# Kernel optimization log

Hardware: AMD Instinct MI355X
Metric: run time of the kernel (lower is better)

## Reference

```python
import jax, jax.numpy as jnp
import numpy as np

B, C, H, W, K = 32, 256, 32, 32, 1024
BETA = 0.25

def setup_inputs() -> dict:
    key = jax.random.key(0)
    k1, k2 = jax.random.split(key)
    z = jax.random.normal(k1, (B, C, H, W), dtype=jnp.float32)
    # torch init: uniform(-1/K, 1/K)
    embedding = jax.random.uniform(k2, (K, C), dtype=jnp.float32,
                                   minval=-1.0 / K, maxval=1.0 / K)
    return {"z": z, "embedding": embedding}

def reference(z, embedding):
    b, c, h, w = z.shape
    k = embedding.shape[0]
    # permute to [b,h,w,c] (contiguous)
    z_p = jnp.transpose(z, (0, 2, 3, 1))
    # Faithful to the torch code: the [b,h,w,c] contiguous buffer is .view()'d
    # as [b,1,c,h,w]; numpy/jnp reshape of the transposed array matches that.
    zz = z_p.reshape(b, c, h * w)                     # [b,c,hw] (reinterpreted)
    e = jax.lax.stop_gradient(embedding)              # torch uses .data here
    # ||e - z||^2 via dot-product trick, avoids [b,k,c,h,w] intermediate
    dist = (jnp.sum(e * e, axis=1)[None, :, None]
            + jnp.sum(zz * zz, axis=1)[:, None, :]
            - 2.0 * jnp.einsum('kc,bcn->bkn', e, zz))  # [b,k,hw]
    idx = jnp.argmin(dist, axis=1).reshape(b, h, w)    # [b,h,w]
    z_q = embedding[idx]                               # [b,h,w,c]
    loss = (jnp.mean((jax.lax.stop_gradient(z_q) - z_p) ** 2)
            + BETA * jnp.mean((z_q - jax.lax.stop_gradient(z_p)) ** 2))
    # straight-through estimator
    z_q_st = z_p + jax.lax.stop_gradient(z_q - z_p)
    return jnp.transpose(z_q_st, (0, 3, 1, 2)), idx, loss
```

## Files before the change

### kernel.cpp

```cpp
#include <hip/hip_runtime.h>
#include <stdint.h>

#define ZSIZE   8388608
#define NPIX    32768
#define IDX_OFF ZSIZE
#define LOSS_OFF (ZSIZE + NPIX)
#define ET_OFF  1024
#define E1_OFF  263168
#define ZT_OFF  394240
#define SZ_OFF  4588544
#define CAP     24
#define WWIN    6.0e-3f

using v8s = __attribute__((ext_vector_type(8))) short;
using v4f = __attribute__((ext_vector_type(4))) float;

__device__ __forceinline__ unsigned short bf16rne(float f) {
  unsigned u = __float_as_uint(f);
  return (unsigned short)((u + 0x7FFFu + ((u >> 16) & 1u)) >> 16);
}

__global__ __launch_bounds__(256) void ktr(const float* __restrict__ E,
                                           float* __restrict__ out) {
  __shared__ float tile[64][65];
  const int k0 = blockIdx.x * 64;
  const int c0 = blockIdx.y * 64;
  const int t = threadIdx.x;
  #pragma unroll
  for (int i = 0; i < 4; i++) {
    int f = t + 256 * i;
    int r = f >> 4, q = f & 15;
    float4 e = *(const float4*)(E + (k0 + r) * 256 + c0 + 4 * q);
    tile[r][4 * q + 0] = e.x; tile[r][4 * q + 1] = e.y;
    tile[r][4 * q + 2] = e.z; tile[r][4 * q + 3] = e.w;
  }
  __syncthreads();
  #pragma unroll
  for (int i = 0; i < 4; i++) {
    int f = t + 256 * i;
    int cr = f >> 4, kq = f & 15;
    float4 o;
    o.x = tile[4 * kq + 0][cr];
    o.y = tile[4 * kq + 1][cr];
    o.z = tile[4 * kq + 2][cr];
    o.w = tile[4 * kq + 3][cr];
    *(float4*)(out + ET_OFF + (c0 + cr) * 1024 + k0 + 4 * kq) = o;
  }
}

__global__ __launch_bounds__(256) void kse(float* __restrict__ out) {
  const int k = blockIdx.x * 256 + threadIdx.x;
  const float* Et = out + ET_OFF;
  float acc = 0.0f;
  #pragma unroll 8
  for (int c = 0; c < 256; c++) {
    float v = Et[c * 1024 + k];
    acc = __fadd_rn(acc, __fmul_rn(v, v));
  }
  out[k] = acc;
}

__global__ __launch_bounds__(256) void kes(const float* __restrict__ E,
                                           float* __restrict__ out) {
  unsigned short* e1s = (unsigned short*)(out + E1_OFF);
  const int tile = blockIdx.x;
  const int t = threadIdx.x;
  #pragma unroll
  for (int i = 0; i < 2; i++) {
    int chunk = t + 256 * i;
    int s = chunk >> 6, lane = chunk & 63;
    int r = lane & 15, h = (lane >> 4) & 3;
    const float* src = E + (16 * tile + r) * 256 + 8 * h + 32 * s;
    unsigned short o[8];
    #pragma unroll
    for (int j = 0; j < 8; j++) o[j] = bf16rne(src[j]);
    *(uint4*)(e1s + (size_t)tile * 4096 + (size_t)chunk * 8) = *(const uint4*)o;
  }
}

__global__ __launch_bounds__(256) void kzt(const float* __restrict__ z,
                                           float* __restrict__ out) {
  __shared__ float tile[16][1028];
  unsigned short* zt = (unsigned short*)(out + ZT_OFF);
  float* szg = out + SZ_OFF;
  const int mg = blockIdx.x;
  const int b  = blockIdx.y;
  const int t = threadIdx.x;
  #pragma unroll
  for (int i = 0; i < 16; i++) {
    float4 v = *(const float4*)(z + (size_t)b * 262144 + (size_t)(mg * 16 + i) * 1024 + 4 * t);
    *(float4*)&tile[i][4 * t] = v;
  }
  __syncthreads();
  const int m = t & 15, w0 = (t >> 4) & 3;
  const int n = w0 * 256 + mg * 16 + m;
  #pragma unroll
  for (int i = 0; i < 8; i++) {
    int g = 4 * i + (t >> 6);
    int c0 = 8 * g;
    unsigned short o[8];
    #pragma unroll
    for (int j = 0; j < 8; j++)
      o[j] = bf16rne(tile[m][4 * (c0 + j) + w0]);
    *(uint4*)(zt + ((size_t)(b * 1024 + n)) * 256 + c0) = *(const uint4*)o;
  }
  if (t < 64) {
    const int ms = t >> 2, ws = t & 3;
    float a = 0.0f;
    #pragma unroll 8
    for (int c = 0; c < 256; c++) {
      float v = tile[ms][4 * c + ws];
      a = __fadd_rn(a, __fmul_rn(v, v));
    }
    szg[b * 1024 + ws * 256 + mg * 16 + ms] = a;
  }
}

__global__ __launch_bounds__(512, 2) void kmain(const float* __restrict__ z,
                                                const float* __restrict__ E,
                                                float* __restrict__ out) {
  __shared__ __attribute__((aligned(16))) float szs[64];
  __shared__ __attribute__((aligned(16))) float dmins[64];
  __shared__ int   candK[64 * CAP];
  __shared__ float candD[64 * CAP];
  __shared__ int   cnt[64];

  const int t = threadIdx.x;
  const int ccg = blockIdx.x, b = blockIdx.y;
  const int cc0 = ccg * 16;
  const int lane = t & 63;
  const int w = (t >> 6) & 3;
  const int Tp = t >> 8;
  const int r = t & 15, h = (t >> 4) & 3;
  const int w16r = w * 16 + r;
  const float* zb = z + (size_t)b * 262144;
  const float* se_g = out;
  const unsigned short* e1s = (const unsigned short*)(out + E1_OFF);
  const unsigned short* zt = (const unsigned short*)(out + ZT_OFF);
  const float* szg = out + SZ_OFF;

  if (t < 64) {
    cnt[t] = 0; dmins[t] = 3.4e38f;
    szs[t] = szg[b * 1024 + (t & 3) * 256 + cc0 + (t >> 2)];
  }
  __syncthreads();

  float se16r[16];
  #pragma unroll
  for (int ti = 0; ti < 16; ti++) se16r[ti] = se_g[ti * 64 + w16r];

  const int T0 = 2 * Tp, T1 = T0 + 1;

  v8s A0[8], A1[8];
  {
    const unsigned short* a0p =
        zt + ((size_t)(b * 1024 + T0 * 256 + cc0 + r)) * 256 + 8 * h;
    const unsigned short* a1p = a0p + 256 * 256;
    #pragma unroll
    for (int s = 0; s < 8; s++) {
      A0[s] = *(const v8s*)(a0p + 32 * s);
      A1[s] = *(const v8s*)(a1p + 32 * s);
    }
  }
  float sz0[4], sz1[4];
  #pragma unroll
  for (int reg = 0; reg < 4; reg++) {
    sz0[reg] = szs[16 * h + 4 * reg + T0];
    sz1[reg] = szs[16 * h + 4 * reg + T1];
  }

  {
    float b0[4], b1[4];
    #pragma unroll
    for (int reg = 0; reg < 4; reg++) { b0[reg] = 3.4e38f; b1[reg] = 3.4e38f; }

    #pragma unroll 4
    for (int ti = 0; ti < 16; ti++) {
      const unsigned short* bb = e1s + (size_t)(4 * ti + w) * 4096 + (size_t)lane * 8;
      v4f acc0 = (v4f){0.f, 0.f, 0.f, 0.f};
      v4f acc1 = (v4f){0.f, 0.f, 0.f, 0.f};
      #pragma unroll
      for (int s = 0; s < 8; s++) {
        v8s B_ = *(const v8s*)(bb + 512 * s);
        acc0 = __builtin_amdgcn_mfma_f32_16x16x32_bf16(A0[s], B_, acc0, 0, 0, 0);
        acc1 = __builtin_amdgcn_mfma_f32_16x16x32_bf16(A1[s], B_, acc1, 0, 0, 0);
      }
      float se_l = se16r[ti];
      #pragma unroll
      for (int reg = 0; reg < 4; reg++) {
        b0[reg] = fminf(b0[reg], (se_l + sz0[reg]) - 2.0f * acc0[reg]);
        b1[reg] = fminf(b1[reg], (se_l + sz1[reg]) - 2.0f * acc1[reg]);
      }
    }
    #pragma unroll
    for (int reg = 0; reg < 4; reg++) {
      atomicMin((int*)&dmins[16 * h + 4 * reg + T0], __float_as_int(b0[reg]));
      atomicMin((int*)&dmins[16 * h + 4 * reg + T1], __float_as_int(b1[reg]));
    }
  }
  __syncthreads();

  {
    float th0[4], th1[4];
    #pragma unroll
    for (int reg = 0; reg < 4; reg++) {
      th0[reg] = dmins[16 * h + 4 * reg + T0] + WWIN;
      th1[reg] = dmins[16 * h + 4 * reg + T1] + WWIN;
    }

    #pragma unroll 4
    for (int ti = 0; ti < 16; ti++) {
      const unsigned short* bb = e1s + (size_t)(4 * ti + w) * 4096 + (size_t)lane * 8;
      v4f acc0 = (v4f){0.f, 0.f, 0.f, 0.f};
      v4f acc1 = (v4f){0.f, 0.f, 0.f, 0.f};
      #pragma unroll
      for (int s = 0; s < 8; s++) {
        v8s B_ = *(const v8s*)(bb + 512 * s);
        acc0 = __builtin_amdgcn_mfma_f32_16x16x32_bf16(A0[s], B_, acc0, 0, 0, 0);
        acc1 = __builtin_amdgcn_mfma_f32_16x16x32_bf16(A1[s], B_, acc1, 0, 0, 0);
      }
      float se_l = se16r[ti];
      const int kl = ti * 64 + w16r;
      #pragma unroll
      for (int reg = 0; reg < 4; reg++) {
        float dd0 = (se_l + sz0[reg]) - 2.0f * acc0[reg];
        if (dd0 <= th0[reg]) {
          int p = 16 * h + 4 * reg + T0;
          int o = atomicAdd(&cnt[p], 1);
          if (o < CAP) { candK[p * CAP + o] = kl; candD[p * CAP + o] = dd0; }
        }
        float dd1 = (se_l + sz1[reg]) - 2.0f * acc1[reg];
        if (dd1 <= th1[reg]) {
          int p = 16 * h + 4 * reg + T1;
          int o = atomicAdd(&cnt[p], 1);
          if (o < CAP) { candK[p * CAP + o] = kl; candD[p * CAP + o] = dd1; }
        }
      }
    }
  }
  __syncthreads();

  for (int i = t; i < 64 * CAP; i += 512) {
    int p = i / CAP, slot = i - p * CAP;
    int cn = cnt[p];
    if (cn > CAP || slot >= cn) continue;
    int k = candK[i];
    const float* er = E + (size_t)k * 256;
    const float* zp = zb + (cc0 + (p >> 2)) * 1024 + (p & 3);
    float dot = 0.0f;
    #pragma unroll 8
    for (int c = 0; c < 256; c++)
      dot = __fmaf_rn(zp[4 * c], er[c], dot);
    candD[i] = __fsub_rn(__fadd_rn(se_g[k], szs[p]), __fmul_rn(2.0f, dot));
  }
  __syncthreads();

  if (t < 64) {
    int p = t, cn = cnt[p];
    if (cn <= CAP) {
      float bd = 3.4e38f; int bi = 0x7FFFFFFF;
      for (int s2 = 0; s2 < cn; s2++) {
        float d2 = candD[p * CAP + s2]; int k2 = candK[p * CAP + s2];
        if (d2 < bd || (d2 == bd && k2 < bi)) { bd = d2; bi = k2; }
      }
      int rr = p >> 2, w0 = p & 3;
      out[IDX_OFF + b * 1024 + (w0 * 256 + cc0 + rr)] = (float)bi;
    }
  }

  for (int p = 0; p < 64; p++) {
    if (cnt[p] > CAP && (p & 3) == w && Tp == 0) {
      const float* zp = zb + (cc0 + (p >> 2)) * 1024 + (p & 3);
      float bd = 3.4e38f; int bi = 0x7FFFFFFF;
      for (int k = lane; k < 1024; k += 64) {
        const float* er = E + (size_t)k * 256;
        float dot = 0.0f;
        #pragma unroll 8
        for (int c = 0; c < 256; c++)
          dot = __fmaf_rn(zp[4 * c], er[c], dot);
        float d2 = __fsub_rn(__fadd_rn(se_g[k], szs[p]), __fmul_rn(2.0f, dot));
        if (d2 < bd || (d2 == bd && k < bi)) { bd = d2; bi = k; }
      }
      #pragma unroll
      for (int mm = 32; mm >= 1; mm >>= 1) {
        float d2 = __shfl_xor(bd, mm, 64);
        int i2 = __shfl_xor(bi, mm, 64);
        if (d2 < bd || (d2 == bd && i2 < bi)) { bd = d2; bi = i2; }
      }
      if (lane == 0) {
        int rr = p >> 2, w0 = p & 3;
        out[IDX_OFF + b * 1024 + (w0 * 256 + cc0 + rr)] = (float)bi;
      }
    }
  }
}

__global__ __launch_bounds__(256) void kout(const float* __restrict__ z,
                                            const float* __restrict__ E,
                                            float* __restrict__ out,
                                            float* __restrict__ ws) {
  __shared__ float red[4];
  const int t = threadIdx.x;
  const size_t g4 = (size_t)blockIdx.x * 256 + t;
  const size_t g = g4 * 4;
  const int b = (int)(g >> 18);
  const int c = (int)((g >> 10) & 255);
  const int n = (int)(g & 1023);

  float4 zp = *(const float4*)(z + g);
  float4 idxf = *(const float4*)(out + IDX_OFF + b * 1024 + n);
  int i0 = (int)idxf.x, i1 = (int)idxf.y, i2 = (int)idxf.z, i3 = (int)idxf.w;
  float q0 = E[i0 * 256 + c];
  float q1 = E[i1 * 256 + c];
  float q2 = E[i2 * 256 + c];
  float q3 = E[i3 * 256 + c];
  float d0 = __fsub_rn(q0, zp.x);
  float d1 = __fsub_rn(q1, zp.y);
  float d2 = __fsub_rn(q2, zp.z);
  float d3 = __fsub_rn(q3, zp.w);
  float4 o;
  o.x = __fadd_rn(zp.x, d0);
  o.y = __fadd_rn(zp.y, d1);
  o.z = __fadd_rn(zp.z, d2);
  o.w = __fadd_rn(zp.w, d3);
  *(float4*)(out + g) = o;

  float s = d0 * d0 + d1 * d1 + d2 * d2 + d3 * d3;
  #pragma unroll
  for (int off = 32; off > 0; off >>= 1) s += __shfl_down(s, off);
  if ((t & 63) == 0) red[t >> 6] = s;
  __syncthreads();
  if (t == 0) ws[blockIdx.x] = red[0] + red[1] + red[2] + red[3];
}

__global__ __launch_bounds__(256) void kfin(const float* __restrict__ ws,
                                            float* __restrict__ out) {
  __shared__ float red[4];
  const int t = threadIdx.x;
  float s = 0.0f;
  #pragma unroll
  for (int i = 0; i < 32; i++) s += ws[t + 256 * i];
  #pragma unroll
  for (int off = 32; off > 0; off >>= 1) s += __shfl_down(s, off);
  if ((t & 63) == 0) red[t >> 6] = s;
  __syncthreads();
  if (t == 0) {
    float S = red[0] + red[1] + red[2] + red[3];
    float m = S / 8388608.0f;
    out[LOSS_OFF] = __fadd_rn(m, __fmul_rn(0.25f, m));
  }
}

extern "C" void kernel_launch(void* const* d_in, const int* in_sizes, int n_in,
                              void* d_out, int out_size, void* d_ws, size_t ws_size,
                              hipStream_t stream) {
  const float* z = (const float*)d_in[0];
  const float* E = (const float*)d_in[1];
  float* out = (float*)d_out;
  float* ws = (float*)d_ws;

  ktr<<<dim3(16, 4), 256, 0, stream>>>(E, out);
  kse<<<dim3(4), 256, 0, stream>>>(out);
  kes<<<dim3(64), 256, 0, stream>>>(E, out);
  kzt<<<dim3(16, 32), 256, 0, stream>>>(z, out);
  kmain<<<dim3(16, 32), 512, 0, stream>>>(z, E, out);
  kout<<<dim3(8192), 256, 0, stream>>>(z, E, out, ws);
  kfin<<<dim3(1), 256, 0, stream>>>(ws, out);
}
```

Before: 305.5 us.

## Cache quantized distances in LDS instead of recomputing MFMA pass for candidate filtering

The main VQ kernel previously ran the bf16 MFMA distance GEMM twice, once for the per-pixel minimum and once to collect candidates. It now stores each distance, minus the pixel norm and quantized to 16 bits, into a large LDS array during the first pass, then filters candidates from those cached values after the min reduction. Each block drops to 256 threads and loops over the two pixel-pair groups, and the codebook tile order is rotated per block to spread L2 traffic. This removes half the MFMA and codebook-load work, but adds about 66KB of LDS per block, which may limit occupancy, and adds quantization error covered by an extra margin.

```diff
diff --git a/kernel.cpp b/kernel.cpp
--- a/kernel.cpp
+++ b/kernel.cpp
@@ -11,6 +11,7 @@
 #define SZ_OFF  4588544
 #define CAP     24
 #define WWIN    6.0e-3f
+#define QMARG   1.5e-4f
 
 using v8s = __attribute__((ext_vector_type(8))) short;
 using v4f = __attribute__((ext_vector_type(4))) float;
@@ -116,23 +117,23 @@
   }
 }
 
-__global__ __launch_bounds__(512, 2) void kmain(const float* __restrict__ z,
+__global__ __launch_bounds__(256, 2) void kmain(const float* __restrict__ z,
                                                 const float* __restrict__ E,
                                                 float* __restrict__ out) {
+  __shared__ __attribute__((aligned(16))) unsigned ddq[256][65];
   __shared__ __attribute__((aligned(16))) float szs[64];
   __shared__ __attribute__((aligned(16))) float dmins[64];
-  __shared__ int   candK[64 * CAP];
+  __shared__ unsigned short candK[64 * CAP];
   __shared__ float candD[64 * CAP];
   __shared__ int   cnt[64];
 
   const int t = threadIdx.x;
   const int ccg = blockIdx.x, b = blockIdx.y;
   const int cc0 = ccg * 16;
-  const int lane = t & 63;
-  const int w = (t >> 6) & 3;
-  const int Tp = t >> 8;
+  const int lane = t & 63, w = t >> 6;
   const int r = t & 15, h = (t >> 4) & 3;
   const int w16r = w * 16 + r;
+  const int perm = (ccg + 2 * b) & 15;
   const float* zb = z + (size_t)b * 262144;
   const float* se_g = out;
   const unsigned short* e1s = (const unsigned short*)(out + E1_OFF);
@@ -145,38 +146,32 @@
   }
   __syncthreads();
 
-  float se16r[16];
-  #pragma unroll
-  for (int ti = 0; ti < 16; ti++) se16r[ti] = se_g[ti * 64 + w16r];
-
-  const int T0 = 2 * Tp, T1 = T0 + 1;
-
-  v8s A0[8], A1[8];
-  {
-    const unsigned short* a0p =
-        zt + ((size_t)(b * 1024 + T0 * 256 + cc0 + r)) * 256 + 8 * h;
-    const unsigned short* a1p = a0p + 256 * 256;
-    #pragma unroll
-    for (int s = 0; s < 8; s++) {
-      A0[s] = *(const v8s*)(a0p + 32 * s);
-      A1[s] = *(const v8s*)(a1p + 32 * s);
-    }
-  }
-  float sz0[4], sz1[4];
-  #pragma unroll
-  for (int reg = 0; reg < 4; reg++) {
-    sz0[reg] = szs[16 * h + 4 * reg + T0];
-    sz1[reg] = szs[16 * h + 4 * reg + T1];
-  }
-
-  {
-    float b0[4], b1[4];
-    #pragma unroll
-    for (int reg = 0; reg < 4; reg++) { b0[reg] = 3.4e38f; b1[reg] = 3.4e38f; }
+  #pragma unroll 1
+  for (int Tp = 0; Tp < 2; Tp++) {
+    const int T0 = 2 * Tp, T1 = T0 + 1;
+    v8s A0[8], A1[8];
+    {
+      const unsigned short* a0p =
+          zt + ((size_t)(b * 1024 + T0 * 256 + cc0 + r)) * 256 + 8 * h;
+      const unsigned short* a1p = a0p + 256 * 256;
+      #pragma unroll
+      for (int s = 0; s < 8; s++) {
+        A0[s] = *(const v8s*)(a0p + 32 * s);
+        A1[s] = *(const v8s*)(a1p + 32 * s);
+      }
+    }
+    float sz0[4], sz1[4], b0[4], b1[4];
+    #pragma unroll
+    for (int reg = 0; reg < 4; reg++) {
+      sz0[reg] = szs[16 * h + 4 * reg + T0];
+      sz1[reg] = szs[16 * h + 4 * reg + T1];
+      b0[reg] = 3.4e38f; b1[reg] = 3.4e38f;
+    }
 
     #pragma unroll 4
     for (int ti = 0; ti < 16; ti++) {
-      const unsigned short* bb = e1s + (size_t)(4 * ti + w) * 4096 + (size_t)lane * 8;
+      const int tj = (ti + perm) & 15;
+      const unsigned short* bb = e1s + (size_t)(4 * tj + w) * 4096 + (size_t)lane * 8;
       v4f acc0 = (v4f){0.f, 0.f, 0.f, 0.f};
       v4f acc1 = (v4f){0.f, 0.f, 0.f, 0.f};
       #pragma unroll
@@ -185,62 +180,59 @@
         acc0 = __builtin_amdgcn_mfma_f32_16x16x32_bf16(A0[s], B_, acc0, 0, 0, 0);
         acc1 = __builtin_amdgcn_mfma_f32_16x16x32_bf16(A1[s], B_, acc1, 0, 0, 0);
       }
-      float se_l = se16r[ti];
+      float se_l = se_g[tj * 64 + w16r];
       #pragma unroll
       for (int reg = 0; reg < 4; reg++) {
-        b0[reg] = fminf(b0[reg], (se_l + sz0[reg]) - 2.0f * acc0[reg]);
-        b1[reg] = fminf(b1[reg], (se_l + sz1[reg]) - 2.0f * acc1[reg]);
-      }
-    }
+        float dd0 = (se_l + sz0[reg]) - 2.0f * acc0[reg];
+        float dd1 = (se_l + sz1[reg]) - 2.0f * acc1[reg];
+        b0[reg] = fminf(b0[reg], dd0);
+        b1[reg] = fminf(b1[reg], dd1);
+        float f0 = dd0 - sz0[reg], f1 = dd1 - sz1[reg];
+        int q0 = (int)((f0 + 1.0f) * 32768.0f);
+        int q1 = (int)((f1 + 1.0f) * 32768.0f);
+        q0 = q0 < 0 ? 0 : (q0 > 65535 ? 65535 : q0);
+        q1 = q1 < 0 ? 0 : (q1 > 65535 ? 65535 : q1);
+        ddq[t][4 * ti + reg] = (unsigned)q0 | ((unsigned)q1 << 16);
+      }
+    }
+
     #pragma unroll
     for (int reg = 0; reg < 4; reg++) {
       atomicMin((int*)&dmins[16 * h + 4 * reg + T0], __float_as_int(b0[reg]));
       atomicMin((int*)&dmins[16 * h + 4 * reg + T1], __float_as_int(b1[reg]));
     }
-  }
-  __syncthreads();
-
-  {
+    __syncthreads();
+
     float th0[4], th1[4];
     #pragma unroll
     for (int reg = 0; reg < 4; reg++) {
-      th0[reg] = dmins[16 * h + 4 * reg + T0] + WWIN;
-      th1[reg] = dmins[16 * h + 4 * reg + T1] + WWIN;
-    }
-
+      th0[reg] = (dmins[16 * h + 4 * reg + T0] + WWIN) - sz0[reg] + QMARG;
+      th1[reg] = (dmins[16 * h + 4 * reg + T1] + WWIN) - sz1[reg] + QMARG;
+    }
     #pragma unroll 4
     for (int ti = 0; ti < 16; ti++) {
-      const unsigned short* bb = e1s + (size_t)(4 * ti + w) * 4096 + (size_t)lane * 8;
-      v4f acc0 = (v4f){0.f, 0.f, 0.f, 0.f};
-      v4f acc1 = (v4f){0.f, 0.f, 0.f, 0.f};
-      #pragma unroll
-      for (int s = 0; s < 8; s++) {
-        v8s B_ = *(const v8s*)(bb + 512 * s);
-        acc0 = __builtin_amdgcn_mfma_f32_16x16x32_bf16(A0[s], B_, acc0, 0, 0, 0);
-        acc1 = __builtin_amdgcn_mfma_f32_16x16x32_bf16(A1[s], B_, acc1, 0, 0, 0);
-      }
-      float se_l = se16r[ti];
-      const int kl = ti * 64 + w16r;
+      const int kl = ((ti + perm) & 15) * 64 + w16r;
       #pragma unroll
       for (int reg = 0; reg < 4; reg++) {
-        float dd0 = (se_l + sz0[reg]) - 2.0f * acc0[reg];
-        if (dd0 <= th0[reg]) {
+        unsigned qd = ddq[t][4 * ti + reg];
+        float f0 = (float)(qd & 0xFFFFu) * (1.0f / 32768.0f) - 1.0f;
+        float f1 = (float)(qd >> 16) * (1.0f / 32768.0f) - 1.0f;
+        if (f0 <= th0[reg]) {
           int p = 16 * h + 4 * reg + T0;
           int o = atomicAdd(&cnt[p], 1);
-          if (o < CAP) { candK[p * CAP + o] = kl; candD[p * CAP + o] = dd0; }
+          if (o < CAP) candK[p * CAP + o] = (unsigned short)kl;
         }
-        float dd1 = (se_l + sz1[reg]) - 2.0f * acc1[reg];
-        if (dd1 <= th1[reg]) {
+        if (f1 <= th1[reg]) {
           int p = 16 * h + 4 * reg + T1;
           int o = atomicAdd(&cnt[p], 1);
-          if (o < CAP) { candK[p * CAP + o] = kl; candD[p * CAP + o] = dd1; }
+          if (o < CAP) candK[p * CAP + o] = (unsigned short)kl;
         }
       }
     }
-  }
-  __syncthreads();
-
-  for (int i = t; i < 64 * CAP; i += 512) {
+    __syncthreads();
+  }
+
+  for (int i = t; i < 64 * CAP; i += 256) {
     int p = i / CAP, slot = i - p * CAP;
     int cn = cnt[p];
     if (cn > CAP || slot >= cn) continue;
@@ -269,7 +261,7 @@
   }
 
   for (int p = 0; p < 64; p++) {
-    if (cnt[p] > CAP && (p & 3) == w && Tp == 0) {
+    if (cnt[p] > CAP && (p & 3) == w) {
       const float* zp = zb + (cc0 + (p >> 2)) * 1024 + (p & 3);
       float bd = 3.4e38f; int bi = 0x7FFFFFFF;
       for (int k = lane; k < 1024; k += 64) {
@@ -363,7 +355,7 @@
   kse<<<dim3(4), 256, 0, stream>>>(out);
   kes<<<dim3(64), 256, 0, stream>>>(E, out);
   kzt<<<dim3(16, 32), 256, 0, stream>>>(z, out);
-  kmain<<<dim3(16, 32), 512, 0, stream>>>(z, E, out);
+  kmain<<<dim3(16, 32), 256, 0, stream>>>(z, E, out);
   kout<<<dim3(8192), 256, 0, stream>>>(z, E, out, ws);
   kfin<<<dim3(1), 256, 0, stream>>>(ws, out);
 }
```

After: 262.0 us. -14.2%, faster.
